# Kernel optimization log

Hardware: AMD Instinct MI355X
Metric: run time of the kernel (lower is better)

## Reference

```python
import jax, jax.numpy as jnp
import numpy as np

N_NODES = 50000
N_EDGES = 800000
D_IN = 64
D_OUT = 64


def setup_inputs() -> dict:
    key = jax.random.key(0)
    k1, k2, k3, k4 = jax.random.split(key, 4)
    x = jax.random.normal(k1, (N_NODES, D_IN), dtype=jnp.float32)
    src = jax.random.randint(k2, (N_EDGES,), 0, N_NODES, dtype=jnp.int64)
    dst = jax.random.randint(k3, (N_EDGES,), 0, N_NODES, dtype=jnp.int64)
    W = jax.random.normal(k4, (D_IN, D_OUT), dtype=jnp.float32) / np.sqrt(D_IN)
    b = jnp.zeros((D_OUT,), dtype=jnp.float32)
    return {"x": x, "src": src, "dst": dst, "W": W, "b": b}


def reference(x, src, dst, W, b):
    # DGL GraphConv, norm='both': out = D_in^{-1/2} A D_out^{-1/2} x W + b
    n = x.shape[0]
    ones = jnp.ones(src.shape[0], dtype=x.dtype)
    out_deg = jax.ops.segment_sum(ones, src, num_segments=n)  # out-degree of each node
    in_deg = jax.ops.segment_sum(ones, dst, num_segments=n)   # in-degree of each node
    norm_src = jax.lax.rsqrt(jnp.clip(out_deg, 1.0))          # [N]
    norm_dst = jax.lax.rsqrt(jnp.clip(in_deg, 1.0))           # [N]
    h = x * norm_src[:, None]                                 # [N, D_in]
    msg = jnp.take(h, src, axis=0)                            # [E, D_in] gather
    agg = jax.ops.segment_sum(msg, dst, num_segments=n)       # [N, D_in] scatter-add
    agg = agg * norm_dst[:, None]
    return agg @ W + b                                        # [N, D_out]
```

## Files before the change

kernel.cpp:

```cpp
#include <hip/hip_runtime.h>
#include <hip/hip_fp16.h>

#define N_NODES 50000
#define N_EDGES 800000
#define D 64

#define SLICES 80
#define I4S (N_EDGES / 4 / SLICES)
#define NWORDS 12512

typedef float vfloat2 __attribute__((ext_vector_type(2)));

#define CTR_OFF    0
#define BASE_OFF   256
#define END_OFF    200320
#define SNORM_OFF  400384
#define DNORM_OFF  600448
#define SSRC_OFF   800512
#define PART_OFF   4000768
#define Y16_OFF    PART_OFF

__global__ __launch_bounds__(256) void degree_lds_kernel(const int4* __restrict__ src4,
                                                         const int4* __restrict__ dst4,
                                                         unsigned int* __restrict__ partial,
                                                         int* __restrict__ ctr) {
    __shared__ unsigned int hist[NWORDS];
    int tid = threadIdx.x;
    if (blockIdx.x == 0 && tid == 0) *ctr = 0;
    uint4* h4 = (uint4*)hist;
    for (int i = tid; i < NWORDS / 4; i += 256) h4[i] = make_uint4(0, 0, 0, 0);
    __syncthreads();

    int role  = blockIdx.x & 1;
    int slice = blockIdx.x >> 1;
    const int4* e = role ? dst4 : src4;
    int beg = slice * I4S, end = beg + I4S;
    for (int i = beg + tid; i < end; i += 256) {
        int4 v = e[i];
        atomicAdd(&hist[v.x >> 2], 1u << ((v.x & 3) * 8));
        atomicAdd(&hist[v.y >> 2], 1u << ((v.y & 3) * 8));
        atomicAdd(&hist[v.z >> 2], 1u << ((v.z & 3) * 8));
        atomicAdd(&hist[v.w >> 2], 1u << ((v.w & 3) * 8));
    }
    __syncthreads();

    uint4* p4 = (uint4*)(partial + (size_t)blockIdx.x * NWORDS);
    for (int i = tid; i < NWORDS / 4; i += 256) p4[i] = h4[i];
}

__global__ __launch_bounds__(256) void merge_scan_kernel(unsigned int* __restrict__ partial,
                                                         int* __restrict__ base,
                                                         int* __restrict__ rend,
                                                         float* __restrict__ snorm,
                                                         float* __restrict__ dnorm,
                                                         int* __restrict__ ctr) {
    int w = blockIdx.x * blockDim.x + threadIdx.x;
    int lane = threadIdx.x & 63;
    unsigned int accin = 0, accout = 0;
    if (w < 12500) {
        unsigned int* po = partial + w;
        unsigned int* pd = partial + NWORDS + w;
#pragma unroll 4
        for (int s = 0; s < SLICES; s++) {
            size_t off = (size_t)(2 * s) * NWORDS;
            accout += po[off];
            unsigned int v = pd[off];
            pd[off] = accin;
            accin += v;
        }
    }
    int d0 = accin & 0xFF, d1 = (accin >> 8) & 0xFF,
        d2 = (accin >> 16) & 0xFF, d3 = (accin >> 24) & 0xFF;
    int tsum = d0 + d1 + d2 + d3;
    int run = tsum;
#pragma unroll
    for (int off = 1; off < 64; off <<= 1) {
        int v = __shfl_up(run, off);
        if (lane >= off) run += v;
    }
    int wtot = __shfl(run, 63);
    int wbase = 0;
    if (lane == 63) wbase = atomicAdd(ctr, wtot);
    wbase = __shfl(wbase, 63);
    if (w < 12500) {
        int b0 = wbase + run - tsum;
        int b1 = b0 + d0, b2 = b1 + d1, b3 = b2 + d2;
        ((int4*)base)[w] = make_int4(b0, b1, b2, b3);
        ((int4*)rend)[w] = make_int4(b1, b2, b3, b3 + d3);
        ((float4*)dnorm)[w] = make_float4(rsqrtf(fmaxf((float)d0, 1.f)),
                                          rsqrtf(fmaxf((float)d1, 1.f)),
                                          rsqrtf(fmaxf((float)d2, 1.f)),
                                          rsqrtf(fmaxf((float)d3, 1.f)));
        int o0 = accout & 0xFF, o1 = (accout >> 8) & 0xFF,
            o2 = (accout >> 16) & 0xFF, o3 = (accout >> 24) & 0xFF;
        ((float4*)snorm)[w] = make_float4(rsqrtf(fmaxf((float)o0, 1.f)),
                                          rsqrtf(fmaxf((float)o1, 1.f)),
                                          rsqrtf(fmaxf((float)o2, 1.f)),
                                          rsqrtf(fmaxf((float)o3, 1.f)));
    }
}

__global__ __launch_bounds__(256) void fill_kernel(const int4* __restrict__ src4,
                                                   const int4* __restrict__ dst4,
                                                   const unsigned int* __restrict__ partial,
                                                   const int* __restrict__ base,
                                                   int* __restrict__ ssrc) {
    __shared__ unsigned int hist[NWORDS];
    int tid = threadIdx.x;
    uint4* h4 = (uint4*)hist;
    for (int i = tid; i < NWORDS / 4; i += 256) h4[i] = make_uint4(0, 0, 0, 0);
    __syncthreads();

    int s = blockIdx.x;
    const int4* sp = src4 + (size_t)s * I4S;
    const int4* dp = dst4 + (size_t)s * I4S;
    const unsigned int* pref = partial + (size_t)(2 * s + 1) * NWORDS;

    for (int i = tid; i < I4S; i += 256) {
        int4 sv = sp[i], tv = dp[i];
#define FILL_ONE(T, S)                                                        \
        {                                                                     \
            int t = (T); int sh = (t & 3) * 8;                                \
            unsigned int old = atomicAdd(&hist[t >> 2], 1u << sh);            \
            int local = (old >> sh) & 0xFF;                                   \
            int p = base[t] + (int)((pref[t >> 2] >> sh) & 0xFFu) + local;    \
            ssrc[p] = (S);                                                    \
        }
        FILL_ONE(tv.x, sv.x)
        FILL_ONE(tv.y, sv.y)
        FILL_ONE(tv.z, sv.z)
        FILL_ONE(tv.w, sv.w)
#undef FILL_ONE
    }
}

#define YBLK 1024
__global__ __launch_bounds__(256, 4) void y_kernel(const float* __restrict__ x,
                                                   const float* __restrict__ snorm,
                                                   const float* __restrict__ W,
                                                   __half* __restrict__ y16) {
    int lane = threadIdx.x & 63;
    int wave = (blockIdx.x << 2) | (threadIdx.x >> 6);

    float Wreg[D];
#pragma unroll
    for (int k = 0; k < D; k++) Wreg[k] = W[k * D + lane];

    for (int n = wave; n < N_NODES; n += YBLK * 4) {
        float hv = x[(size_t)n * D + lane] * snorm[n];
        int hb = __float_as_int(hv);
        float p0 = 0.f, p1 = 0.f, p2 = 0.f, p3 = 0.f;
#pragma unroll
        for (int k = 0; k < D; k += 4) {
            p0 = fmaf(__int_as_float(__builtin_amdgcn_readlane(hb, k + 0)), Wreg[k + 0], p0);
            p1 = fmaf(__int_as_float(__builtin_amdgcn_readlane(hb, k + 1)), Wreg[k + 1], p1);
            p2 = fmaf(__int_as_float(__builtin_amdgcn_readlane(hb, k + 2)), Wreg[k + 2], p2);
            p3 = fmaf(__int_as_float(__builtin_amdgcn_readlane(hb, k + 3)), Wreg[k + 3], p3);
        }
        y16[(size_t)n * D + lane] = __float2half((p0 + p1) + (p2 + p3));
    }
}

#define GBLK 2048
__global__ __launch_bounds__(256, 8) void gather_kernel(const __half2* __restrict__ y2,
                                                        const int* __restrict__ ssrc,
                                                        const int* __restrict__ base,
                                                        const int* __restrict__ rend,
                                                        const float* __restrict__ dnorm,
                                                        const float* __restrict__ b,
                                                        float* __restrict__ out) {
    int lane = threadIdx.x & 63;
    int half = lane & 1;
    int col  = lane >> 1;
    int wave = (blockIdx.x << 2) | (threadIdx.x >> 6);

    float2 b2 = ((const float2*)b)[col];
    const __half2* yl = y2 + col;

    for (int n = wave; n < N_NODES; n += GBLK * 4) {
        int beg = base[n], end = rend[n];
        float ax0 = 0.f, ay0 = 0.f, ax1 = 0.f, ay1 = 0.f;
        float ax2 = 0.f, ay2 = 0.f, ax3 = 0.f, ay3 = 0.f;
        float ax4 = 0.f, ay4 = 0.f, ax5 = 0.f, ay5 = 0.f;
        float ax6 = 0.f, ay6 = 0.f, ax7 = 0.f, ay7 = 0.f;
        int i0 = beg;
        for (; i0 + 16 <= end; i0 += 16) {
            int e = i0 + half;
            int s0 = ssrc[e],      s1 = ssrc[e + 2],  s2 = ssrc[e + 4],  s3 = ssrc[e + 6];
            int s4 = ssrc[e + 8],  s5 = ssrc[e + 10], s6 = ssrc[e + 12], s7 = ssrc[e + 14];
            float2 f0 = __half22float2(yl[(size_t)s0 * 32]);
            float2 f1 = __half22float2(yl[(size_t)s1 * 32]);
            float2 f2 = __half22float2(yl[(size_t)s2 * 32]);
            float2 f3 = __half22float2(yl[(size_t)s3 * 32]);
            float2 f4 = __half22float2(yl[(size_t)s4 * 32]);
            float2 f5 = __half22float2(yl[(size_t)s5 * 32]);
            float2 f6 = __half22float2(yl[(size_t)s6 * 32]);
            float2 f7 = __half22float2(yl[(size_t)s7 * 32]);
            ax0 += f0.x; ay0 += f0.y; ax1 += f1.x; ay1 += f1.y;
            ax2 += f2.x; ay2 += f2.y; ax3 += f3.x; ay3 += f3.y;
            ax4 += f4.x; ay4 += f4.y; ax5 += f5.x; ay5 += f5.y;
            ax6 += f6.x; ay6 += f6.y; ax7 += f7.x; ay7 += f7.y;
        }
        for (; i0 + 2 <= end; i0 += 2) {
            int s = ssrc[i0 + half];
            float2 f = __half22float2(yl[(size_t)s * 32]);
            ax0 += f.x; ay0 += f.y;
        }
        if (i0 < end && half == 0) {
            int s = ssrc[i0];
            float2 f = __half22float2(yl[(size_t)s * 32]);
            ax1 += f.x; ay1 += f.y;
        }
        float sx = ((ax0 + ax1) + (ax2 + ax3)) + ((ax4 + ax5) + (ax6 + ax7));
        float sy = ((ay0 + ay1) + (ay2 + ay3)) + ((ay4 + ay5) + (ay6 + ay7));
        sx += __shfl(sx, lane ^ 1);
        sy += __shfl(sy, lane ^ 1);
        if (half == 0) {
            float dn = dnorm[n];
            vfloat2 o;
            o.x = fmaf(sx, dn, b2.x);
            o.y = fmaf(sy, dn, b2.y);
            __builtin_nontemporal_store(o, (vfloat2*)(out + (size_t)n * D) + col);
        }
    }
}

extern "C" void kernel_launch(void* const* d_in, const int* in_sizes, int n_in,
                              void* d_out, int out_size, void* d_ws, size_t ws_size,
                              hipStream_t stream) {
    const float* x   = (const float*)d_in[0];
    const int*   src = (const int*)d_in[1];
    const int*   dst = (const int*)d_in[2];
    const float* W   = (const float*)d_in[3];
    const float* b   = (const float*)d_in[4];
    float* out = (float*)d_out;

    char* ws = (char*)d_ws;
    int*          ctr   = (int*)(ws + CTR_OFF);
    int*          base  = (int*)(ws + BASE_OFF);
    int*          rend  = (int*)(ws + END_OFF);
    float*        snorm = (float*)(ws + SNORM_OFF);
    float*        dnorm = (float*)(ws + DNORM_OFF);
    int*          ssrc  = (int*)(ws + SSRC_OFF);
    unsigned int* part  = (unsigned int*)(ws + PART_OFF);
    __half*       y16   = (__half*)(ws + Y16_OFF);

    degree_lds_kernel<<<2 * SLICES, 256, 0, stream>>>((const int4*)src,
                                                      (const int4*)dst, part, ctr);
    merge_scan_kernel<<<(12500 + 255) / 256, 256, 0, stream>>>(part, base, rend,
                                                               snorm, dnorm, ctr);
    fill_kernel<<<SLICES, 256, 0, stream>>>((const int4*)src, (const int4*)dst,
                                            part, base, ssrc);
    y_kernel<<<YBLK, 256, 0, stream>>>(x, snorm, W, y16);
    gather_kernel<<<GBLK, 256, 0, stream>>>((const __half2*)y16, ssrc, base, rend,
                                            dnorm, b, out);
}
```

Measured before the change: 161.9 us.

## Fuse merge, fill, projection and gather into one cooperative kernel with grid syncs

The degree pass now records each edge's within-slice occurrence rank in a byte buffer. That lets the fill phase drop its LDS histogram and run fully parallel across the grid instead of in 80 serial slice blocks. Merge/scan, fill plus the projection, and gather are fused into a single cooperative kernel separated by grid.sync, which removes several launch gaps. Separate kernels remain as a fallback if the cooperative launch fails. The gather is also rewritten so each lane loads 4 halves (8 bytes) and four edges are processed in parallel per wave, at the cost of grid-wide barriers and a 1024-block persistent grid.

```diff
diff --git a/kernel.cpp b/kernel.cpp
--- a/kernel.cpp
+++ b/kernel.cpp
@@ -1,15 +1,20 @@
 #include <hip/hip_runtime.h>
 #include <hip/hip_fp16.h>
+#include <hip/hip_cooperative_groups.h>
+
+namespace cg = cooperative_groups;
 
 #define N_NODES 50000
 #define N_EDGES 800000
 #define D 64
 
-#define SLICES 80
-#define I4S (N_EDGES / 4 / SLICES)
+#define SLICES 100
+#define I4S    2000
+#define NI4    200000
 #define NWORDS 12512
-
-typedef float vfloat2 __attribute__((ext_vector_type(2)));
+#define GRID   1024
+
+typedef float vfloat4 __attribute__((ext_vector_type(4)));
 
 #define CTR_OFF    0
 #define BASE_OFF   256
@@ -17,12 +22,14 @@
 #define SNORM_OFF  400384
 #define DNORM_OFF  600448
 #define SSRC_OFF   800512
-#define PART_OFF   4000768
-#define Y16_OFF    PART_OFF
-
-__global__ __launch_bounds__(256) void degree_lds_kernel(const int4* __restrict__ src4,
+#define OCC_OFF    4000768
+#define PART_OFF   4800768
+#define Y16_OFF    14810368
+
+__global__ __launch_bounds__(256) void degree_occ_kernel(const int4* __restrict__ src4,
                                                          const int4* __restrict__ dst4,
                                                          unsigned int* __restrict__ partial,
+                                                         uchar4* __restrict__ occ4,
                                                          int* __restrict__ ctr) {
     __shared__ unsigned int hist[NWORDS];
     int tid = threadIdx.x;
@@ -33,14 +40,25 @@
 
     int role  = blockIdx.x & 1;
     int slice = blockIdx.x >> 1;
-    const int4* e = role ? dst4 : src4;
     int beg = slice * I4S, end = beg + I4S;
-    for (int i = beg + tid; i < end; i += 256) {
-        int4 v = e[i];
-        atomicAdd(&hist[v.x >> 2], 1u << ((v.x & 3) * 8));
-        atomicAdd(&hist[v.y >> 2], 1u << ((v.y & 3) * 8));
-        atomicAdd(&hist[v.z >> 2], 1u << ((v.z & 3) * 8));
-        atomicAdd(&hist[v.w >> 2], 1u << ((v.w & 3) * 8));
+    if (role == 0) {
+        for (int i = beg + tid; i < end; i += 256) {
+            int4 v = src4[i];
+            atomicAdd(&hist[v.x >> 2], 1u << ((v.x & 3) * 8));
+            atomicAdd(&hist[v.y >> 2], 1u << ((v.y & 3) * 8));
+            atomicAdd(&hist[v.z >> 2], 1u << ((v.z & 3) * 8));
+            atomicAdd(&hist[v.w >> 2], 1u << ((v.w & 3) * 8));
+        }
+    } else {
+        for (int i = beg + tid; i < end; i += 256) {
+            int4 v = dst4[i];
+            unsigned int o0 = (atomicAdd(&hist[v.x >> 2], 1u << ((v.x & 3) * 8)) >> ((v.x & 3) * 8)) & 0xFFu;
+            unsigned int o1 = (atomicAdd(&hist[v.y >> 2], 1u << ((v.y & 3) * 8)) >> ((v.y & 3) * 8)) & 0xFFu;
+            unsigned int o2 = (atomicAdd(&hist[v.z >> 2], 1u << ((v.z & 3) * 8)) >> ((v.z & 3) * 8)) & 0xFFu;
+            unsigned int o3 = (atomicAdd(&hist[v.w >> 2], 1u << ((v.w & 3) * 8)) >> ((v.w & 3) * 8)) & 0xFFu;
+            occ4[i] = make_uchar4((unsigned char)o0, (unsigned char)o1,
+                                  (unsigned char)o2, (unsigned char)o3);
+        }
     }
     __syncthreads();
 
@@ -48,16 +66,18 @@
     for (int i = tid; i < NWORDS / 4; i += 256) p4[i] = h4[i];
 }
 
-__global__ __launch_bounds__(256) void merge_scan_kernel(unsigned int* __restrict__ partial,
-                                                         int* __restrict__ base,
-                                                         int* __restrict__ rend,
-                                                         float* __restrict__ snorm,
-                                                         float* __restrict__ dnorm,
-                                                         int* __restrict__ ctr) {
-    int w = blockIdx.x * blockDim.x + threadIdx.x;
-    int lane = threadIdx.x & 63;
+
+__device__ __forceinline__ void phase_merge(unsigned int* __restrict__ partial,
+                                            int* __restrict__ base,
+                                            int* __restrict__ rend,
+                                            float* __restrict__ snorm,
+                                            float* __restrict__ dnorm,
+                                            int* __restrict__ ctr,
+                                            int tid, int lane) {
+    int w = tid;
     unsigned int accin = 0, accout = 0;
-    if (w < 12500) {
+    bool act = (w < 12500);
+    if (act) {
         unsigned int* po = partial + w;
         unsigned int* pd = partial + NWORDS + w;
 #pragma unroll 4
@@ -80,9 +100,9 @@
     }
     int wtot = __shfl(run, 63);
     int wbase = 0;
-    if (lane == 63) wbase = atomicAdd(ctr, wtot);
+    if (lane == 63 && wtot != 0) wbase = atomicAdd(ctr, wtot);
     wbase = __shfl(wbase, 63);
-    if (w < 12500) {
+    if (act) {
         int b0 = wbase + run - tsum;
         int b1 = b0 + d0, b2 = b1 + d1, b3 = b2 + d2;
         ((int4*)base)[w] = make_int4(b0, b1, b2, b3);
@@ -100,53 +120,42 @@
     }
 }
 
-__global__ __launch_bounds__(256) void fill_kernel(const int4* __restrict__ src4,
-                                                   const int4* __restrict__ dst4,
-                                                   const unsigned int* __restrict__ partial,
-                                                   const int* __restrict__ base,
-                                                   int* __restrict__ ssrc) {
-    __shared__ unsigned int hist[NWORDS];
-    int tid = threadIdx.x;
-    uint4* h4 = (uint4*)hist;
-    for (int i = tid; i < NWORDS / 4; i += 256) h4[i] = make_uint4(0, 0, 0, 0);
-    __syncthreads();
-
-    int s = blockIdx.x;
-    const int4* sp = src4 + (size_t)s * I4S;
-    const int4* dp = dst4 + (size_t)s * I4S;
-    const unsigned int* pref = partial + (size_t)(2 * s + 1) * NWORDS;
-
-    for (int i = tid; i < I4S; i += 256) {
-        int4 sv = sp[i], tv = dp[i];
-#define FILL_ONE(T, S)                                                        \
+__device__ __forceinline__ void phase_fill(const int4* __restrict__ src4,
+                                           const int4* __restrict__ dst4,
+                                           const uchar4* __restrict__ occ4,
+                                           const unsigned int* __restrict__ partial,
+                                           const int* __restrict__ base,
+                                           int* __restrict__ ssrc,
+                                           int tid) {
+    if (tid < NI4) {
+        int s = tid / I4S;
+        const unsigned int* pref = partial + (size_t)(2 * s + 1) * NWORDS;
+        int4 sv = src4[tid], tv = dst4[tid];
+        uchar4 oc = occ4[tid];
+#define FILL_ONE(T, S, O)                                                     \
         {                                                                     \
             int t = (T); int sh = (t & 3) * 8;                                \
-            unsigned int old = atomicAdd(&hist[t >> 2], 1u << sh);            \
-            int local = (old >> sh) & 0xFF;                                   \
-            int p = base[t] + (int)((pref[t >> 2] >> sh) & 0xFFu) + local;    \
+            int p = base[t] + (int)((pref[t >> 2] >> sh) & 0xFFu) + (int)(O); \
             ssrc[p] = (S);                                                    \
         }
-        FILL_ONE(tv.x, sv.x)
-        FILL_ONE(tv.y, sv.y)
-        FILL_ONE(tv.z, sv.z)
-        FILL_ONE(tv.w, sv.w)
+        FILL_ONE(tv.x, sv.x, oc.x)
+        FILL_ONE(tv.y, sv.y, oc.y)
+        FILL_ONE(tv.z, sv.z, oc.z)
+        FILL_ONE(tv.w, sv.w, oc.w)
 #undef FILL_ONE
     }
 }
 
-#define YBLK 1024
-__global__ __launch_bounds__(256, 4) void y_kernel(const float* __restrict__ x,
-                                                   const float* __restrict__ snorm,
-                                                   const float* __restrict__ W,
-                                                   __half* __restrict__ y16) {
-    int lane = threadIdx.x & 63;
-    int wave = (blockIdx.x << 2) | (threadIdx.x >> 6);
-
+__device__ __forceinline__ void phase_y(const float* __restrict__ x,
+                                        const float* __restrict__ snorm,
+                                        const float* __restrict__ W,
+                                        __half* __restrict__ y16,
+                                        int tid, int lane, int nwaves) {
     float Wreg[D];
 #pragma unroll
     for (int k = 0; k < D; k++) Wreg[k] = W[k * D + lane];
-
-    for (int n = wave; n < N_NODES; n += YBLK * 4) {
+    int wave = tid >> 6;
+    for (int n = wave; n < N_NODES; n += nwaves) {
         float hv = x[(size_t)n * D + lane] * snorm[n];
         int hb = __float_as_int(hv);
         float p0 = 0.f, p1 = 0.f, p2 = 0.f, p3 = 0.f;
@@ -161,68 +170,120 @@
     }
 }
 
-#define GBLK 2048
-__global__ __launch_bounds__(256, 8) void gather_kernel(const __half2* __restrict__ y2,
-                                                        const int* __restrict__ ssrc,
-                                                        const int* __restrict__ base,
-                                                        const int* __restrict__ rend,
-                                                        const float* __restrict__ dnorm,
-                                                        const float* __restrict__ b,
-                                                        float* __restrict__ out) {
+__device__ __forceinline__ void phase_gather(const __half* __restrict__ y16,
+                                             const int* __restrict__ ssrc,
+                                             const int* __restrict__ base,
+                                             const int* __restrict__ rend,
+                                             const float* __restrict__ dnorm,
+                                             const float* __restrict__ bias,
+                                             float* __restrict__ out,
+                                             int tid, int lane, int nwaves) {
+    int quad = lane >> 4;
+    int c    = lane & 15;
+    int wave = tid >> 6;
+    float4 b4 = ((const float4*)bias)[c];
+    const uint2* ycol = (const uint2*)y16 + c;
+
+#define ACC(A, V)                                                             \
+    {                                                                         \
+        __half2 h01 = *(__half2*)&(V).x; __half2 h23 = *(__half2*)&(V).y;     \
+        float2 f01 = __half22float2(h01); float2 f23 = __half22float2(h23);   \
+        (A).x += f01.x; (A).y += f01.y; (A).z += f23.x; (A).w += f23.y;       \
+    }
+
+    for (int n = wave; n < N_NODES; n += nwaves) {
+        int beg = base[n], end = rend[n];
+        float4 a0 = make_float4(0, 0, 0, 0), a1 = a0, a2 = a0, a3 = a0;
+        float4 a4 = a0, a5 = a0, a6 = a0, a7 = a0;
+        int i = beg;
+        for (; i + 32 <= end; i += 32) {
+            int s0 = ssrc[i + quad],      s1 = ssrc[i + 4 + quad];
+            int s2 = ssrc[i + 8 + quad],  s3 = ssrc[i + 12 + quad];
+            int s4 = ssrc[i + 16 + quad], s5 = ssrc[i + 20 + quad];
+            int s6 = ssrc[i + 24 + quad], s7 = ssrc[i + 28 + quad];
+            uint2 v0 = ycol[(size_t)s0 * 16];
+            uint2 v1 = ycol[(size_t)s1 * 16];
+            uint2 v2 = ycol[(size_t)s2 * 16];
+            uint2 v3 = ycol[(size_t)s3 * 16];
+            uint2 v4 = ycol[(size_t)s4 * 16];
+            uint2 v5 = ycol[(size_t)s5 * 16];
+            uint2 v6 = ycol[(size_t)s6 * 16];
+            uint2 v7 = ycol[(size_t)s7 * 16];
+            ACC(a0, v0) ACC(a1, v1) ACC(a2, v2) ACC(a3, v3)
+            ACC(a4, v4) ACC(a5, v5) ACC(a6, v6) ACC(a7, v7)
+        }
+        for (; i + 4 <= end; i += 4) {
+            int s = ssrc[i + quad];
+            uint2 v = ycol[(size_t)s * 16];
+            ACC(a0, v)
+        }
+        if (i + quad < end) {
+            int s = ssrc[i + quad];
+            uint2 v = ycol[(size_t)s * 16];
+            ACC(a1, v)
+        }
+        float4 t;
+        t.x = ((a0.x + a1.x) + (a2.x + a3.x)) + ((a4.x + a5.x) + (a6.x + a7.x));
+        t.y = ((a0.y + a1.y) + (a2.y + a3.y)) + ((a4.y + a5.y) + (a6.y + a7.y));
+        t.z = ((a0.z + a1.z) + (a2.z + a3.z)) + ((a4.z + a5.z) + (a6.z + a7.z));
+        t.w = ((a0.w + a1.w) + (a2.w + a3.w)) + ((a4.w + a5.w) + (a6.w + a7.w));
+        t.x += __shfl(t.x, lane ^ 16); t.y += __shfl(t.y, lane ^ 16);
+        t.z += __shfl(t.z, lane ^ 16); t.w += __shfl(t.w, lane ^ 16);
+        t.x += __shfl(t.x, lane ^ 32); t.y += __shfl(t.y, lane ^ 32);
+        t.z += __shfl(t.z, lane ^ 32); t.w += __shfl(t.w, lane ^ 32);
+        if (quad == 0) {
+            float dn = dnorm[n];
+            vfloat4 o;
+            o.x = fmaf(t.x, dn, b4.x);
+            o.y = fmaf(t.y, dn, b4.y);
+            o.z = fmaf(t.z, dn, b4.z);
+            o.w = fmaf(t.w, dn, b4.w);
+            __builtin_nontemporal_store(o, (vfloat4*)(out + (size_t)n * D) + c);
+        }
+    }
+#undef ACC
+}
+
+__global__ __launch_bounds__(256, 4) void coop_kernel(const int4* src4, const int4* dst4,
+                                                      unsigned int* partial, const uchar4* occ4,
+                                                      int* base, int* rend,
+                                                      float* snorm, float* dnorm, int* ctr,
+                                                      int* ssrc, const float* x, const float* W,
+                                                      __half* y16, const float* bias, float* out) {
+    cg::grid_group grid = cg::this_grid();
+    int tid = blockIdx.x * blockDim.x + threadIdx.x;
     int lane = threadIdx.x & 63;
-    int half = lane & 1;
-    int col  = lane >> 1;
-    int wave = (blockIdx.x << 2) | (threadIdx.x >> 6);
-
-    float2 b2 = ((const float2*)b)[col];
-    const __half2* yl = y2 + col;
-
-    for (int n = wave; n < N_NODES; n += GBLK * 4) {
-        int beg = base[n], end = rend[n];
-        float ax0 = 0.f, ay0 = 0.f, ax1 = 0.f, ay1 = 0.f;
-        float ax2 = 0.f, ay2 = 0.f, ax3 = 0.f, ay3 = 0.f;
-        float ax4 = 0.f, ay4 = 0.f, ax5 = 0.f, ay5 = 0.f;
-        float ax6 = 0.f, ay6 = 0.f, ax7 = 0.f, ay7 = 0.f;
-        int i0 = beg;
-        for (; i0 + 16 <= end; i0 += 16) {
-            int e = i0 + half;
-            int s0 = ssrc[e],      s1 = ssrc[e + 2],  s2 = ssrc[e + 4],  s3 = ssrc[e + 6];
-            int s4 = ssrc[e + 8],  s5 = ssrc[e + 10], s6 = ssrc[e + 12], s7 = ssrc[e + 14];
-            float2 f0 = __half22float2(yl[(size_t)s0 * 32]);
-            float2 f1 = __half22float2(yl[(size_t)s1 * 32]);
-            float2 f2 = __half22float2(yl[(size_t)s2 * 32]);
-            float2 f3 = __half22float2(yl[(size_t)s3 * 32]);
-            float2 f4 = __half22float2(yl[(size_t)s4 * 32]);
-            float2 f5 = __half22float2(yl[(size_t)s5 * 32]);
-            float2 f6 = __half22float2(yl[(size_t)s6 * 32]);
-            float2 f7 = __half22float2(yl[(size_t)s7 * 32]);
-            ax0 += f0.x; ay0 += f0.y; ax1 += f1.x; ay1 += f1.y;
-            ax2 += f2.x; ay2 += f2.y; ax3 += f3.x; ay3 += f3.y;
-            ax4 += f4.x; ay4 += f4.y; ax5 += f5.x; ay5 += f5.y;
-            ax6 += f6.x; ay6 += f6.y; ax7 += f7.x; ay7 += f7.y;
-        }
-        for (; i0 + 2 <= end; i0 += 2) {
-            int s = ssrc[i0 + half];
-            float2 f = __half22float2(yl[(size_t)s * 32]);
-            ax0 += f.x; ay0 += f.y;
-        }
-        if (i0 < end && half == 0) {
-            int s = ssrc[i0];
-            float2 f = __half22float2(yl[(size_t)s * 32]);
-            ax1 += f.x; ay1 += f.y;
-        }
-        float sx = ((ax0 + ax1) + (ax2 + ax3)) + ((ax4 + ax5) + (ax6 + ax7));
-        float sy = ((ay0 + ay1) + (ay2 + ay3)) + ((ay4 + ay5) + (ay6 + ay7));
-        sx += __shfl(sx, lane ^ 1);
-        sy += __shfl(sy, lane ^ 1);
-        if (half == 0) {
-            float dn = dnorm[n];
-            vfloat2 o;
-            o.x = fmaf(sx, dn, b2.x);
-            o.y = fmaf(sy, dn, b2.y);
-            __builtin_nontemporal_store(o, (vfloat2*)(out + (size_t)n * D) + col);
-        }
-    }
+    int nwaves = (gridDim.x * blockDim.x) >> 6;
+
+    phase_merge(partial, base, rend, snorm, dnorm, ctr, tid, lane);
+    grid.sync();
+    phase_fill(src4, dst4, occ4, partial, base, ssrc, tid);
+    phase_y(x, snorm, W, y16, tid, lane, nwaves);
+    grid.sync();
+    phase_gather(y16, ssrc, base, rend, dnorm, bias, out, tid, lane, nwaves);
+}
+
+__global__ __launch_bounds__(256, 4) void merge_fb(unsigned int* partial, int* base, int* rend,
+                                                   float* snorm, float* dnorm, int* ctr) {
+    int tid = blockIdx.x * blockDim.x + threadIdx.x;
+    phase_merge(partial, base, rend, snorm, dnorm, ctr, tid, threadIdx.x & 63);
+}
+__global__ __launch_bounds__(256, 4) void filly_fb(const int4* src4, const int4* dst4,
+                                                   const uchar4* occ4, unsigned int* partial,
+                                                   int* base, int* ssrc, const float* x,
+                                                   const float* snorm, const float* W, __half* y16) {
+    int tid = blockIdx.x * blockDim.x + threadIdx.x;
+    int nwaves = (gridDim.x * blockDim.x) >> 6;
+    phase_fill(src4, dst4, occ4, partial, base, ssrc, tid);
+    phase_y(x, snorm, W, y16, tid, threadIdx.x & 63, nwaves);
+}
+__global__ __launch_bounds__(256, 4) void gather_fb(const __half* y16, const int* ssrc,
+                                                    const int* base, const int* rend,
+                                                    const float* dnorm, const float* bias,
+                                                    float* out) {
+    int tid = blockIdx.x * blockDim.x + threadIdx.x;
+    int nwaves = (gridDim.x * blockDim.x) >> 6;
+    phase_gather(y16, ssrc, base, rend, dnorm, bias, out, tid, threadIdx.x & 63, nwaves);
 }
 
 extern "C" void kernel_launch(void* const* d_in, const int* in_sizes, int n_in,
@@ -242,16 +303,25 @@
     float*        snorm = (float*)(ws + SNORM_OFF);
     float*        dnorm = (float*)(ws + DNORM_OFF);
     int*          ssrc  = (int*)(ws + SSRC_OFF);
+    uchar4*       occ4  = (uchar4*)(ws + OCC_OFF);
     unsigned int* part  = (unsigned int*)(ws + PART_OFF);
     __half*       y16   = (__half*)(ws + Y16_OFF);
 
-    degree_lds_kernel<<<2 * SLICES, 256, 0, stream>>>((const int4*)src,
-                                                      (const int4*)dst, part, ctr);
-    merge_scan_kernel<<<(12500 + 255) / 256, 256, 0, stream>>>(part, base, rend,
-                                                               snorm, dnorm, ctr);
-    fill_kernel<<<SLICES, 256, 0, stream>>>((const int4*)src, (const int4*)dst,
-                                            part, base, ssrc);
-    y_kernel<<<YBLK, 256, 0, stream>>>(x, snorm, W, y16);
-    gather_kernel<<<GBLK, 256, 0, stream>>>((const __half2*)y16, ssrc, base, rend,
-                                            dnorm, b, out);
-}
+    const int4* src4 = (const int4*)src;
+    const int4* dst4 = (const int4*)dst;
+
+    degree_occ_kernel<<<2 * SLICES, 256, 0, stream>>>(src4, dst4, part, occ4, ctr);
+
+    void* args[] = {(void*)&src4, (void*)&dst4, (void*)&part, (void*)&occ4,
+                    (void*)&base, (void*)&rend, (void*)&snorm, (void*)&dnorm,
+                    (void*)&ctr, (void*)&ssrc, (void*)&x, (void*)&W,
+                    (void*)&y16, (void*)&b, (void*)&out};
+    hipError_t e = hipLaunchCooperativeKernel((const void*)coop_kernel,
+                                              dim3(GRID), dim3(256), args, 0, stream);
+    if (e != hipSuccess) {
+        merge_fb<<<GRID, 256, 0, stream>>>(part, base, rend, snorm, dnorm, ctr);
+        filly_fb<<<GRID, 256, 0, stream>>>(src4, dst4, occ4, part, base, ssrc,
+                                           x, snorm, W, y16);
+        gather_fb<<<GRID, 256, 0, stream>>>(y16, ssrc, base, rend, dnorm, b, out);
+    }
+}
```

Result: slower. 409.4 us (+152.9%).

## Record per-edge slice offsets in degree pass and fuse CSR fill with y transform

Applied to the files above, without the earlier changes.

The degree kernel's destination-role blocks now save the pre-increment byte of each LDS atomic as a per-edge occurrence offset. The fill step can then compute CSR positions without redoing LDS atomics, so it runs as a fully parallel one-thread-per-int4 pass. That fill is merged into the y (xW) kernel to remove a launch and to spread the previously 80-block serial fill across 1024 blocks. Slices go from 80 to 100, and the workspace layout moves to hold an extra 800KB occupancy buffer and avoid aliasing y16 with the partials.

```diff
diff --git a/kernel.cpp b/kernel.cpp
--- a/kernel.cpp
+++ b/kernel.cpp
@@ -5,8 +5,9 @@
 #define N_EDGES 800000
 #define D 64
 
-#define SLICES 80
-#define I4S (N_EDGES / 4 / SLICES)
+#define SLICES 100
+#define I4S    2000
+#define NI4    200000
 #define NWORDS 12512
 
 typedef float vfloat2 __attribute__((ext_vector_type(2)));
@@ -17,12 +18,14 @@
 #define SNORM_OFF  400384
 #define DNORM_OFF  600448
 #define SSRC_OFF   800512
-#define PART_OFF   4000768
-#define Y16_OFF    PART_OFF
-
-__global__ __launch_bounds__(256) void degree_lds_kernel(const int4* __restrict__ src4,
+#define OCC_OFF    4000768
+#define PART_OFF   4800768
+#define Y16_OFF    14810368
+
+__global__ __launch_bounds__(256) void degree_occ_kernel(const int4* __restrict__ src4,
                                                          const int4* __restrict__ dst4,
                                                          unsigned int* __restrict__ partial,
+                                                         uchar4* __restrict__ occ4,
                                                          int* __restrict__ ctr) {
     __shared__ unsigned int hist[NWORDS];
     int tid = threadIdx.x;
@@ -33,14 +36,25 @@
 
     int role  = blockIdx.x & 1;
     int slice = blockIdx.x >> 1;
-    const int4* e = role ? dst4 : src4;
     int beg = slice * I4S, end = beg + I4S;
-    for (int i = beg + tid; i < end; i += 256) {
-        int4 v = e[i];
-        atomicAdd(&hist[v.x >> 2], 1u << ((v.x & 3) * 8));
-        atomicAdd(&hist[v.y >> 2], 1u << ((v.y & 3) * 8));
-        atomicAdd(&hist[v.z >> 2], 1u << ((v.z & 3) * 8));
-        atomicAdd(&hist[v.w >> 2], 1u << ((v.w & 3) * 8));
+    if (role == 0) {
+        for (int i = beg + tid; i < end; i += 256) {
+            int4 v = src4[i];
+            atomicAdd(&hist[v.x >> 2], 1u << ((v.x & 3) * 8));
+            atomicAdd(&hist[v.y >> 2], 1u << ((v.y & 3) * 8));
+            atomicAdd(&hist[v.z >> 2], 1u << ((v.z & 3) * 8));
+            atomicAdd(&hist[v.w >> 2], 1u << ((v.w & 3) * 8));
+        }
+    } else {
+        for (int i = beg + tid; i < end; i += 256) {
+            int4 v = dst4[i];
+            unsigned int o0 = (atomicAdd(&hist[v.x >> 2], 1u << ((v.x & 3) * 8)) >> ((v.x & 3) * 8)) & 0xFFu;
+            unsigned int o1 = (atomicAdd(&hist[v.y >> 2], 1u << ((v.y & 3) * 8)) >> ((v.y & 3) * 8)) & 0xFFu;
+            unsigned int o2 = (atomicAdd(&hist[v.z >> 2], 1u << ((v.z & 3) * 8)) >> ((v.z & 3) * 8)) & 0xFFu;
+            unsigned int o3 = (atomicAdd(&hist[v.w >> 2], 1u << ((v.w & 3) * 8)) >> ((v.w & 3) * 8)) & 0xFFu;
+            occ4[i] = make_uchar4((unsigned char)o0, (unsigned char)o1,
+                                  (unsigned char)o2, (unsigned char)o3);
+        }
     }
     __syncthreads();
 
@@ -100,53 +114,44 @@
     }
 }
 
-__global__ __launch_bounds__(256) void fill_kernel(const int4* __restrict__ src4,
-                                                   const int4* __restrict__ dst4,
-                                                   const unsigned int* __restrict__ partial,
-                                                   const int* __restrict__ base,
-                                                   int* __restrict__ ssrc) {
-    __shared__ unsigned int hist[NWORDS];
-    int tid = threadIdx.x;
-    uint4* h4 = (uint4*)hist;
-    for (int i = tid; i < NWORDS / 4; i += 256) h4[i] = make_uint4(0, 0, 0, 0);
-    __syncthreads();
-
-    int s = blockIdx.x;
-    const int4* sp = src4 + (size_t)s * I4S;
-    const int4* dp = dst4 + (size_t)s * I4S;
-    const unsigned int* pref = partial + (size_t)(2 * s + 1) * NWORDS;
-
-    for (int i = tid; i < I4S; i += 256) {
-        int4 sv = sp[i], tv = dp[i];
-#define FILL_ONE(T, S)                                                        \
+#define FYBLK 1024
+__global__ __launch_bounds__(256, 4) void filly_kernel(const int4* __restrict__ src4,
+                                                       const int4* __restrict__ dst4,
+                                                       const uchar4* __restrict__ occ4,
+                                                       const unsigned int* __restrict__ partial,
+                                                       const int* __restrict__ base,
+                                                       int* __restrict__ ssrc,
+                                                       const float* __restrict__ x,
+                                                       const float* __restrict__ snorm,
+                                                       const float* __restrict__ W,
+                                                       __half* __restrict__ y16) {
+    int tid = blockIdx.x * blockDim.x + threadIdx.x;
+    int lane = threadIdx.x & 63;
+
+    if (tid < NI4) {
+        int s = tid / I4S;
+        const unsigned int* pref = partial + (size_t)(2 * s + 1) * NWORDS;
+        int4 sv = src4[tid], tv = dst4[tid];
+        uchar4 oc = occ4[tid];
+#define FILL_ONE(T, S, O)                                                     \
         {                                                                     \
             int t = (T); int sh = (t & 3) * 8;                                \
-            unsigned int old = atomicAdd(&hist[t >> 2], 1u << sh);            \
-            int local = (old >> sh) & 0xFF;                                   \
-            int p = base[t] + (int)((pref[t >> 2] >> sh) & 0xFFu) + local;    \
+            int p = base[t] + (int)((pref[t >> 2] >> sh) & 0xFFu) + (int)(O); \
             ssrc[p] = (S);                                                    \
         }
-        FILL_ONE(tv.x, sv.x)
-        FILL_ONE(tv.y, sv.y)
-        FILL_ONE(tv.z, sv.z)
-        FILL_ONE(tv.w, sv.w)
+        FILL_ONE(tv.x, sv.x, oc.x)
+        FILL_ONE(tv.y, sv.y, oc.y)
+        FILL_ONE(tv.z, sv.z, oc.z)
+        FILL_ONE(tv.w, sv.w, oc.w)
 #undef FILL_ONE
     }
-}
-
-#define YBLK 1024
-__global__ __launch_bounds__(256, 4) void y_kernel(const float* __restrict__ x,
-                                                   const float* __restrict__ snorm,
-                                                   const float* __restrict__ W,
-                                                   __half* __restrict__ y16) {
-    int lane = threadIdx.x & 63;
-    int wave = (blockIdx.x << 2) | (threadIdx.x >> 6);
 
     float Wreg[D];
 #pragma unroll
     for (int k = 0; k < D; k++) Wreg[k] = W[k * D + lane];
-
-    for (int n = wave; n < N_NODES; n += YBLK * 4) {
+    int wave = tid >> 6;
+    const int nwaves = FYBLK * 4;
+    for (int n = wave; n < N_NODES; n += nwaves) {
         float hv = x[(size_t)n * D + lane] * snorm[n];
         int hb = __float_as_int(hv);
         float p0 = 0.f, p1 = 0.f, p2 = 0.f, p3 = 0.f;
@@ -242,16 +247,18 @@
     float*        snorm = (float*)(ws + SNORM_OFF);
     float*        dnorm = (float*)(ws + DNORM_OFF);
     int*          ssrc  = (int*)(ws + SSRC_OFF);
+    uchar4*       occ4  = (uchar4*)(ws + OCC_OFF);
     unsigned int* part  = (unsigned int*)(ws + PART_OFF);
     __half*       y16   = (__half*)(ws + Y16_OFF);
 
-    degree_lds_kernel<<<2 * SLICES, 256, 0, stream>>>((const int4*)src,
-                                                      (const int4*)dst, part, ctr);
+    const int4* src4 = (const int4*)src;
+    const int4* dst4 = (const int4*)dst;
+
+    degree_occ_kernel<<<2 * SLICES, 256, 0, stream>>>(src4, dst4, part, occ4, ctr);
     merge_scan_kernel<<<(12500 + 255) / 256, 256, 0, stream>>>(part, base, rend,
                                                                snorm, dnorm, ctr);
-    fill_kernel<<<SLICES, 256, 0, stream>>>((const int4*)src, (const int4*)dst,
-                                            part, base, ssrc);
-    y_kernel<<<YBLK, 256, 0, stream>>>(x, snorm, W, y16);
+    filly_kernel<<<FYBLK, 256, 0, stream>>>(src4, dst4, occ4, part, base, ssrc,
+                                            x, snorm, W, y16);
     gather_kernel<<<GBLK, 256, 0, stream>>>((const __half2*)y16, ssrc, base, rend,
                                             dnorm, b, out);
 }
```

After: 151.5 us. -6.4%, faster.
